# Kernel tuning notes

Hardware: AMD Instinct MI355X
Metric: run time of the kernel (lower is better)

The kernel has to match this reference:

```python
import jax, jax.numpy as jnp
import numpy as np

# Voxel grid size from LSS init: x,y,z bounds / (step * project_scale)
NX, NY, NZ = 128, 128, 16


def setup_inputs() -> dict:
    key = jax.random.key(0)
    k1, k2 = jax.random.split(key)
    B, N, D, H, W, C = 1, 6, 112, 16, 44, 80
    x = jax.random.normal(k1, (B, N, D, H, W, C), dtype=jnp.float32)
    # integer voxel coordinates; some out-of-range on purpose (filtered by kept mask)
    geom_feats = jax.random.randint(k2, (B, N, D, H, W, 3), 0, 130, dtype=jnp.int32)
    return {"x": x, "geom_feats": geom_feats}


def reference(x, geom_feats):
    # Faithful JAX version of LSS.voxel_pooling:
    # sort-by-rank + cumsum + diff (QuickCumsum) == segment-sum over voxel ids.
    B = x.shape[0]
    C = x.shape[-1]
    xf = x.reshape(-1, C)                      # [Nprime, C]
    g = geom_feats.reshape(-1, 3)              # [Nprime, 3]
    Nprime = g.shape[0]
    per_b = Nprime // B
    batch_ix = jnp.repeat(jnp.arange(B, dtype=jnp.int32), per_b)

    gx, gy, gz = g[:, 0], g[:, 1], g[:, 2]
    kept = (gx >= 0) & (gx < NX) & (gy >= 0) & (gy < NY) & (gz >= 0) & (gz < NZ)

    nseg = B * NX * NY * NZ
    seg = ((batch_ix * NX + gx) * NY + gy) * NZ + gz
    seg = jnp.where(kept, seg, nseg)           # route invalid points to dummy bucket

    pooled = jax.ops.segment_sum(xf, seg, num_segments=nseg + 1)[:nseg]
    # torch layout: final[b, :, z, x, y]
    final = pooled.reshape(B, NX, NY, NZ, C).transpose(0, 4, 3, 1, 2)  # [B,C,Z,X,Y]
    return final
```

## Files before the change

### kernel.cpp

```cpp
#include <hip/hip_runtime.h>


#define BNX 128
#define BNY 128
#define BNZ 16
#define BC  80
#define PLANE      (BNX * BNY)
#define NSEG_PER_B (BNZ * PLANE)
#define ZX         (BNZ * BNX)
#define CCAP 16
#define GT 512

typedef float fvec4 __attribute__((ext_vector_type(4)));

__global__ __launch_bounds__(256) void init_cnt(int4* __restrict__ cnt4, int n4)
{
    int i = blockIdx.x * blockDim.x + threadIdx.x;
    if (i < n4) cnt4[i] = make_int4(0, 0, 0, 0);
}

__global__ __launch_bounds__(256) void fill_cells(
    const int* __restrict__ geom,
    int* __restrict__ cellcnt,
    int* __restrict__ celllist,
    int npoints, int per_b)
{
    int p = blockIdx.x * blockDim.x + threadIdx.x;
    if (p >= npoints) return;

    int gx = geom[p * 3 + 0];
    int gy = geom[p * 3 + 1];
    int gz = geom[p * 3 + 2];
    if ((unsigned)gx >= (unsigned)BNX ||
        (unsigned)gy >= (unsigned)BNY ||
        (unsigned)gz >= (unsigned)BNZ) return;

    int b    = p / per_b;
    int cell = ((b * BNZ + gz) * BNX + gx) * BNY + gy;
    int pos  = atomicAdd(&cellcnt[cell], 1);
    if (pos < CCAP) celllist[(size_t)cell * CCAP + pos] = p;
}

__global__ __launch_bounds__(GT) void gather_csr(
    const float* __restrict__ x,
    const int* __restrict__ cellcnt,
    const int* __restrict__ celllist,
    float* __restrict__ out)
{
    const int tid = threadIdx.x;
    const int cs  = tid >> 7;
    const int y   = tid & 127;
    const int row = blockIdx.x;
    const int b   = row >> 11;
    const int zx  = row & (ZX - 1);

    const int cell = row * BNY + y;
    int m = cellcnt[cell];
    m = m < CCAP ? m : CCAP;

    fvec4 a0 = {0,0,0,0}, a1 = {0,0,0,0}, a2 = {0,0,0,0},
          a3 = {0,0,0,0}, a4 = {0,0,0,0};

    const int* cl = &celllist[(size_t)cell * CCAP];
    for (int k = 0; k < m; ++k) {
        int p = cl[k];
        const fvec4* xr = reinterpret_cast<const fvec4*>(
            &x[(size_t)p * BC + cs * 20]);
        a0 += xr[0]; a1 += xr[1]; a2 += xr[2]; a3 += xr[3]; a4 += xr[4];
    }

    size_t obase = (size_t)(b * BC + cs * 20) * NSEG_PER_B
                 + (size_t)zx * BNY + y;
    float v[20] = { a0.x,a0.y,a0.z,a0.w, a1.x,a1.y,a1.z,a1.w,
                    a2.x,a2.y,a2.z,a2.w, a3.x,a3.y,a3.z,a3.w,
                    a4.x,a4.y,a4.z,a4.w };
    #pragma unroll
    for (int j = 0; j < 20; ++j)
        out[obase + (size_t)j * NSEG_PER_B] = v[j];
}

extern "C" void kernel_launch(void* const* d_in, const int* in_sizes, int n_in,
                              void* d_out, int out_size, void* d_ws, size_t ws_size,
                              hipStream_t stream)
{
    const float* x  = (const float*)d_in[0];
    const int* geom = (const int*)d_in[1];
    float* out      = (float*)d_out;

    const int npoints = in_sizes[0] / BC;
    const int B       = out_size / (BC * NSEG_PER_B);
    const int per_b   = npoints / (B > 0 ? B : 1);
    const int ncell   = B * NSEG_PER_B;

    int* cellcnt  = (int*)d_ws;
    int* celllist = cellcnt + ncell;

    const int n4 = ncell / 4;
    init_cnt<<<(n4 + 255) / 256, 256, 0, stream>>>((int4*)cellcnt, n4);

    fill_cells<<<(npoints + 255) / 256, 256, 0, stream>>>(
        geom, cellcnt, celllist, npoints, per_b);

    gather_csr<<<B * ZX, GT, 0, stream>>>(x, cellcnt, celllist, out);
}
```

Measured before the change: 33.49 us.

## Pack cell counts into bytes and process four cells per thread with vector stores

Cell counters are packed as 8-bit fields, four to a 32-bit word. This shrinks the count array and its zeroing cost, and fill uses a shifted atomicAdd. The gather kernel now gives each thread four adjacent y cells and 5 channels, skips empty groups of four cells early, and writes float4 vectors to the output. The trade-off is that counts wrap if more than 255 points land in one cell (the carry would corrupt the neighbouring byte), and loads from x become scalar and strided rather than float4.

New measurement: 35.10 us. 1.05x slower.

```diff
diff --git a/kernel.cpp b/kernel.cpp
--- a/kernel.cpp
+++ b/kernel.cpp
@@ -21,7 +21,7 @@
 
 __global__ __launch_bounds__(256) void fill_cells(
     const int* __restrict__ geom,
-    int* __restrict__ cellcnt,
+    unsigned int* __restrict__ cnt32,
     int* __restrict__ celllist,
     int npoints, int per_b)
 {
@@ -37,46 +37,51 @@
 
     int b    = p / per_b;
     int cell = ((b * BNZ + gz) * BNX + gx) * BNY + gy;
-    int pos  = atomicAdd(&cellcnt[cell], 1);
+    int sh   = 8 * (cell & 3);
+    unsigned old = atomicAdd(&cnt32[cell >> 2], 1u << sh);
+    int pos = (int)((old >> sh) & 0xFF);
     if (pos < CCAP) celllist[(size_t)cell * CCAP + pos] = p;
 }
 
 __global__ __launch_bounds__(GT) void gather_csr(
     const float* __restrict__ x,
-    const int* __restrict__ cellcnt,
+    const unsigned int* __restrict__ cnt32,
     const int* __restrict__ celllist,
     float* __restrict__ out)
 {
     const int tid = threadIdx.x;
-    const int cs  = tid >> 7;
-    const int y   = tid & 127;
+    const int g   = tid >> 5;
+    const int q   = tid & 31;
     const int row = blockIdx.x;
     const int b   = row >> 11;
     const int zx  = row & (ZX - 1);
 
-    const int cell = row * BNY + y;
-    int m = cellcnt[cell];
-    m = m < CCAP ? m : CCAP;
+    const unsigned w = cnt32[row * (BNY / 4) + q];
 
-    fvec4 a0 = {0,0,0,0}, a1 = {0,0,0,0}, a2 = {0,0,0,0},
-          a3 = {0,0,0,0}, a4 = {0,0,0,0};
+    float a[4][5] = {};
 
-    const int* cl = &celllist[(size_t)cell * CCAP];
-    for (int k = 0; k < m; ++k) {
-        int p = cl[k];
-        const fvec4* xr = reinterpret_cast<const fvec4*>(
-            &x[(size_t)p * BC + cs * 20]);
-        a0 += xr[0]; a1 += xr[1]; a2 += xr[2]; a3 += xr[3]; a4 += xr[4];
+    if (w != 0) {
+        const int cellbase = row * BNY + 4 * q;
+        #pragma unroll
+        for (int j = 0; j < 4; ++j) {
+            int m = (int)((w >> (8 * j)) & 0xFF);
+            m = m < CCAP ? m : CCAP;
+            const int* cl = &celllist[(size_t)(cellbase + j) * CCAP];
+            for (int k = 0; k < m; ++k) {
+                const float* xr = &x[(size_t)cl[k] * BC + g * 5];
+                #pragma unroll
+                for (int jc = 0; jc < 5; ++jc) a[j][jc] += xr[jc];
+            }
+        }
     }
 
-    size_t obase = (size_t)(b * BC + cs * 20) * NSEG_PER_B
-                 + (size_t)zx * BNY + y;
-    float v[20] = { a0.x,a0.y,a0.z,a0.w, a1.x,a1.y,a1.z,a1.w,
-                    a2.x,a2.y,a2.z,a2.w, a3.x,a3.y,a3.z,a3.w,
-                    a4.x,a4.y,a4.z,a4.w };
+    size_t obase = (size_t)(b * BC + g * 5) * NSEG_PER_B
+                 + (size_t)zx * BNY + 4 * q;
     #pragma unroll
-    for (int j = 0; j < 20; ++j)
-        out[obase + (size_t)j * NSEG_PER_B] = v[j];
+    for (int jc = 0; jc < 5; ++jc) {
+        fvec4 v = { a[0][jc], a[1][jc], a[2][jc], a[3][jc] };
+        *reinterpret_cast<fvec4*>(&out[obase + (size_t)jc * NSEG_PER_B]) = v;
+    }
 }
 
 extern "C" void kernel_launch(void* const* d_in, const int* in_sizes, int n_in,
@@ -92,14 +97,14 @@
     const int per_b   = npoints / (B > 0 ? B : 1);
     const int ncell   = B * NSEG_PER_B;
 
-    int* cellcnt  = (int*)d_ws;
-    int* celllist = cellcnt + ncell;
+    unsigned int* cnt32 = (unsigned int*)d_ws;
+    int* celllist = (int*)(cnt32 + ncell / 4);
 
-    const int n4 = ncell / 4;
-    init_cnt<<<(n4 + 255) / 256, 256, 0, stream>>>((int4*)cellcnt, n4);
+    const int n4 = ncell / 16;
+    init_cnt<<<(n4 + 255) / 256, 256, 0, stream>>>((int4*)cnt32, n4);
 
     fill_cells<<<(npoints + 255) / 256, 256, 0, stream>>>(
-        geom, cellcnt, celllist, npoints, per_b);
+        geom, cnt32, celllist, npoints, per_b);
 
-    gather_csr<<<B * ZX, GT, 0, stream>>>(x, cellcnt, celllist, out);
+    gather_csr<<<B * ZX, GT, 0, stream>>>(x, cnt32, celllist, out);
 }
```
